# Optimization experiments

Measured on AMD Instinct MI355X. Metric: run time of the kernel, lower is better.

## Reference

```python
import jax, jax.numpy as jnp
import numpy as np

N_NODES = 50000


def _add_self_loops(edge_index, num_nodes):
    loop = jnp.arange(num_nodes, dtype=edge_index.dtype)
    row = jnp.concatenate([edge_index[0], loop])
    col = jnp.concatenate([edge_index[1], loop])
    return row, col


def _gcn_norm(row, col, num_nodes):
    # deg computed on target index with unit edge weights (PyG gcn_norm)
    deg = jax.ops.segment_sum(jnp.ones_like(col, dtype=jnp.float32), col,
                              num_segments=num_nodes)
    dis = jnp.where(deg > 0, jax.lax.rsqrt(jnp.maximum(deg, 1.0)), 0.0)
    return dis[row] * dis[col]  # [E]


def _gcn_conv(x, W, b, row, col, norm, num_nodes):
    h = x @ W                                  # dense transform first (PyG order)
    msg = h[row] * norm[:, None]               # gather + normalize
    out = jax.ops.segment_sum(msg, col, num_segments=num_nodes)  # scatter-add
    return out + b


def setup_inputs() -> dict:
    key = jax.random.key(0)
    ks = jax.random.split(key, 10)
    E = 800000
    x = jax.random.normal(ks[0], (N_NODES, 29), dtype=jnp.float32)
    edge_index = jax.random.randint(ks[1], (2, E), 0, N_NODES, dtype=jnp.int64)

    def glorot(k, fan_in, fan_out):
        s = jnp.sqrt(2.0 / (fan_in + fan_out)).astype(jnp.float32)
        return jax.random.normal(k, (fan_in, fan_out), dtype=jnp.float32) * s

    return {
        "x": x, "edge_index": edge_index,
        "W1": glorot(ks[2], 29, 96),  "b1": jnp.zeros((96,), jnp.float32),
        "W2": glorot(ks[3], 96, 128), "b2": jnp.zeros((128,), jnp.float32),
        "W3": glorot(ks[4], 128, 64), "b3": jnp.zeros((64,), jnp.float32),
        "W4": glorot(ks[5], 64, 32),  "b4": jnp.zeros((32,), jnp.float32),
    }


def reference(x, edge_index, W1, b1, W2, b2, W3, b3, W4, b4):
    row, col = _add_self_loops(edge_index, N_NODES)
    norm = _gcn_norm(row, col, N_NODES)  # same graph -> same norm for all layers
    h = _gcn_conv(x, W1, b1, row, col, norm, N_NODES)
    h = jax.nn.relu(h)
    # dropout(p=0.4) is identity in eval mode
    h = _gcn_conv(h, W2, b2, row, col, norm, N_NODES)
    h = _gcn_conv(h, W3, b3, row, col, norm, N_NODES)
    h = _gcn_conv(h, W4, b4, row, col, norm, N_NODES)
    return h
```

## Files before the change

### kernel.cpp

```cpp
#include <hip/hip_runtime.h>


constexpr int NN  = 50000;
constexpr int CAP = 64;
constexpr int AGB = (NN * 8 + 255) / 256;
constexpr int C1B = (NN + 255) / 256;
constexpr int PREPB = (NN * 32 + 64 + 255) / 256;
constexpr int W34XB = 17;
constexpr int W234XB = 13;
constexpr int PGB = 128;
constexpr int SLICE = (800000 + PGB - 1) / PGB;

typedef unsigned short u16;

__global__ void place_x_kernel(const int* __restrict__ row, const int* __restrict__ col,
                               int* __restrict__ cnt, u16* __restrict__ ell, int E) {
    const int g  = blockIdx.x & 7;
    const int bi = blockIdx.x >> 3;
    const int e0 = bi * SLICE;
    int e1 = e0 + SLICE; if (e1 > E) e1 = E;
    for (int e = e0 + threadIdx.x; e < e1; e += 256) {
        const int c = col[e];
        if ((unsigned)c >= (unsigned)NN || ((c >> 6) & 7) != g) continue;
        const int r = row[e];
        if ((unsigned)r >= (unsigned)NN) continue;
        const int pos = atomicAdd(&cnt[c], 1);
        if (pos < CAP) ell[c * CAP + pos] = (u16)r;
    }
}

__global__ void prep_all_kernel(const int* __restrict__ cnt, u16* __restrict__ ell,
                                const float* __restrict__ x, float* __restrict__ dis,
                                float* __restrict__ Ba, float* __restrict__ Bb,
                                float* __restrict__ c1d,
                                const float* __restrict__ W3, const float* __restrict__ W4,
                                const float* __restrict__ b3,
                                float* __restrict__ W34, float* __restrict__ v1) {
    if (blockIdx.x >= PREPB) {
        const int wid = (blockIdx.x - PREPB) * 256 + threadIdx.x;
        if (wid < 4096) {
            const int r = wid >> 5, j = wid & 31;
            float a = 0.f;
#pragma unroll 8
            for (int k = 0; k < 64; ++k) a = fmaf(W3[r * 64 + k], W4[k * 32 + j], a);
            W34[wid] = a;
        } else if (wid < 4128) {
            const int j = wid - 4096;
            float a = 0.f;
#pragma unroll 8
            for (int k = 0; k < 64; ++k) a = fmaf(b3[k], W4[k * 32 + j], a);
            v1[j] = a;
        }
        return;
    }
    const int idx = blockIdx.x * blockDim.x + threadIdx.x;
    if (idx < NN * 32) {
        const int n = idx >> 5, f = idx & 31;
        int m = cnt[n]; if (m > CAP) m = CAP;
        const float d = rsqrtf((float)m + 1.0f);
        Ba[idx] = (f < 29) ? x[n * 29 + f] * d : 0.f;
        if (f == 31) dis[n] = d;
        if (f == 30) {
            int mp = (m + 7) & ~7; if (mp > CAP) mp = CAP;
            for (int k = m; k < mp; ++k) ell[n * CAP + k] = (u16)NN;
        }
    } else {
        const int i = idx - NN * 32;
        if (i < 32) { Ba[NN * 32 + i] = 0.f; Bb[NN * 32 + i] = 0.f; }
        else if (i == 32) dis[NN] = 0.f;
        else if (i == 33) c1d[NN] = 0.f;
    }
}

template<int MODE>
__device__ __forceinline__ void agg32_body(const float* __restrict__ hs,
                                           const int* __restrict__ cnt,
                                           const u16* __restrict__ ell,
                                           const float* __restrict__ dis,
                                           const float* __restrict__ c1,
                                           const float* __restrict__ c2,
                                           const float* __restrict__ v1,
                                           const float* __restrict__ v2,
                                           const float* __restrict__ bv,
                                           float* __restrict__ out) {
    const int idx = blockIdx.x * blockDim.x + threadIdx.x;
    if (idx >= NN * 8) return;
    const int n = idx >> 3, c = idx & 7;
    const float4* hpc = (const float4*)hs + c;
    float4 acc = hpc[n * 8];
    int m = cnt[n]; if (m > CAP) m = CAP;
    const int m8 = (m + 7) >> 3;
    const int4* ip = (const int4*)(ell + (size_t)n * CAP);
    int t = 0;
    for (; t + 2 <= m8; t += 2) {
        const int4 sA = ip[t], sB = ip[t + 1];
        const unsigned ax = (unsigned)sA.x, ay = (unsigned)sA.y;
        const unsigned az = (unsigned)sA.z, aw = (unsigned)sA.w;
        const unsigned bx = (unsigned)sB.x, by = (unsigned)sB.y;
        const unsigned bz = (unsigned)sB.z, bw = (unsigned)sB.w;
        const float4 g0 = hpc[(ax & 0xFFFFu) * 8], g1 = hpc[(ax >> 16) * 8];
        const float4 g2 = hpc[(ay & 0xFFFFu) * 8], g3 = hpc[(ay >> 16) * 8];
        const float4 g4 = hpc[(az & 0xFFFFu) * 8], g5 = hpc[(az >> 16) * 8];
        const float4 g6 = hpc[(aw & 0xFFFFu) * 8], g7 = hpc[(aw >> 16) * 8];
        const float4 h0 = hpc[(bx & 0xFFFFu) * 8], h1 = hpc[(bx >> 16) * 8];
        const float4 h2 = hpc[(by & 0xFFFFu) * 8], h3 = hpc[(by >> 16) * 8];
        const float4 h4 = hpc[(bz & 0xFFFFu) * 8], h5 = hpc[(bz >> 16) * 8];
        const float4 h6 = hpc[(bw & 0xFFFFu) * 8], h7 = hpc[(bw >> 16) * 8];
        acc.x += (((g0.x + g1.x) + (g2.x + g3.x)) + ((g4.x + g5.x) + (g6.x + g7.x)))
               + (((h0.x + h1.x) + (h2.x + h3.x)) + ((h4.x + h5.x) + (h6.x + h7.x)));
        acc.y += (((g0.y + g1.y) + (g2.y + g3.y)) + ((g4.y + g5.y) + (g6.y + g7.y)))
               + (((h0.y + h1.y) + (h2.y + h3.y)) + ((h4.y + h5.y) + (h6.y + h7.y)));
        acc.z += (((g0.z + g1.z) + (g2.z + g3.z)) + ((g4.z + g5.z) + (g6.z + g7.z)))
               + (((h0.z + h1.z) + (h2.z + h3.z)) + ((h4.z + h5.z) + (h6.z + h7.z)));
        acc.w += (((g0.w + g1.w) + (g2.w + g3.w)) + ((g4.w + g5.w) + (g6.w + g7.w)))
               + (((h0.w + h1.w) + (h2.w + h3.w)) + ((h4.w + h5.w) + (h6.w + h7.w)));
    }
    if (t < m8) {
        const int4 s = ip[t];
        const unsigned ux = (unsigned)s.x, uy = (unsigned)s.y;
        const unsigned uz = (unsigned)s.z, uw = (unsigned)s.w;
        const float4 g0 = hpc[(ux & 0xFFFFu) * 8], g1 = hpc[(ux >> 16) * 8];
        const float4 g2 = hpc[(uy & 0xFFFFu) * 8], g3 = hpc[(uy >> 16) * 8];
        const float4 g4 = hpc[(uz & 0xFFFFu) * 8], g5 = hpc[(uz >> 16) * 8];
        const float4 g6 = hpc[(uw & 0xFFFFu) * 8], g7 = hpc[(uw >> 16) * 8];
        acc.x += ((g0.x + g1.x) + (g2.x + g3.x)) + ((g4.x + g5.x) + (g6.x + g7.x));
        acc.y += ((g0.y + g1.y) + (g2.y + g3.y)) + ((g4.y + g5.y) + (g6.y + g7.y));
        acc.z += ((g0.z + g1.z) + (g2.z + g3.z)) + ((g4.z + g5.z) + (g6.z + g7.z));
        acc.w += ((g0.w + g1.w) + (g2.w + g3.w)) + ((g4.w + g5.w) + (g6.w + g7.w));
    }
    const float d = dis[n];
    float4 r;
    if (MODE == 0) {
        r.x = acc.x * d; r.y = acc.y * d; r.z = acc.z * d; r.w = acc.w * d;
    } else if (MODE == 1) {
        const float d2 = d * d;
        r.x = acc.x * d2; r.y = acc.y * d2; r.z = acc.z * d2; r.w = acc.w * d2;
    } else {
        const float a1 = c1[n], a2 = c2[n];
        const float4 w1 = ((const float4*)v1)[c];
        const float4 w2 = ((const float4*)v2)[c];
        const float4 bb = ((const float4*)bv)[c];
        r.x = fmaf(acc.x, d, fmaf(a1, w1.x, fmaf(a2, w2.x, bb.x)));
        r.y = fmaf(acc.y, d, fmaf(a1, w1.y, fmaf(a2, w2.y, bb.y)));
        r.z = fmaf(acc.z, d, fmaf(a1, w1.z, fmaf(a2, w2.z, bb.z)));
        r.w = fmaf(acc.w, d, fmaf(a1, w1.w, fmaf(a2, w2.w, bb.w)));
    }
    ((float4*)out)[idx] = r;
}

__device__ __forceinline__ void agg1_body(const float* __restrict__ in,
                                          const int* __restrict__ cnt,
                                          const u16* __restrict__ ell,
                                          const float* __restrict__ dis,
                                          float* __restrict__ out,
                                          float* __restrict__ outd, int blk0) {
    const int n = (blockIdx.x - blk0) * 256 + threadIdx.x;
    if (n >= NN) return;
    float acc = in[n];
    int m = cnt[n]; if (m > CAP) m = CAP;
    const int m8 = (m + 7) >> 3;
    const int4* ip = (const int4*)(ell + (size_t)n * CAP);
    for (int t = 0; t < m8; ++t) {
        const int4 s = ip[t];
        const unsigned ux = (unsigned)s.x, uy = (unsigned)s.y;
        const unsigned uz = (unsigned)s.z, uw = (unsigned)s.w;
        acc += ((in[ux & 0xFFFFu] + in[ux >> 16]) + (in[uy & 0xFFFFu] + in[uy >> 16]))
             + ((in[uz & 0xFFFFu] + in[uz >> 16]) + (in[uw & 0xFFFFu] + in[uw >> 16]));
    }
    const float r = dis[n] * acc;
    out[n] = r;
    if (outd) outd[n] = r * dis[n];
}

__global__ void agg_pre_kernel(const float* __restrict__ Ba, const int* __restrict__ cnt,
                               const u16* __restrict__ ell, const float* __restrict__ dis,
                               float* __restrict__ Bb, float* __restrict__ c1,
                               float* __restrict__ c1d,
                               const float* __restrict__ W2, const float* __restrict__ b2,
                               const float* __restrict__ W34, float* __restrict__ W234,
                               float* __restrict__ v2) {
    if (blockIdx.x < AGB) {
        agg32_body<0>(Ba, cnt, ell, dis, nullptr, nullptr, nullptr, nullptr, nullptr, Bb);
    } else if (blockIdx.x < AGB + C1B) {
        agg1_body(dis, cnt, ell, dis, c1, c1d, AGB);
    } else {
        const int wid = (blockIdx.x - AGB - C1B) * 256 + threadIdx.x;
        if (wid < 3072) {
            const int r = wid >> 5, j = wid & 31;
            float a = 0.f;
#pragma unroll 8
            for (int k = 0; k < 128; ++k) a = fmaf(W2[r * 128 + k], W34[k * 32 + j], a);
            W234[wid] = a;
        } else if (wid < 3104) {
            const int j = wid - 3072;
            float a = 0.f;
#pragma unroll 8
            for (int k = 0; k < 128; ++k) a = fmaf(b2[k], W34[k * 32 + j], a);
            v2[j] = a;
        }
    }
}

__global__ void agg_hop1_kernel(const float* __restrict__ Ba, const int* __restrict__ cnt,
                                const u16* __restrict__ ell, const float* __restrict__ dis,
                                float* __restrict__ Bb, const float* __restrict__ c1d,
                                float* __restrict__ c2) {
    if (blockIdx.x < AGB)
        agg32_body<1>(Ba, cnt, ell, dis, nullptr, nullptr, nullptr, nullptr, nullptr, Bb);
    else
        agg1_body(c1d, cnt, ell, dis, c2, nullptr, AGB);
}

__global__ void agg_hop2_kernel(const float* __restrict__ Bb, const int* __restrict__ cnt,
                                const u16* __restrict__ ell, const float* __restrict__ dis,
                                float* __restrict__ Ba) {
    agg32_body<1>(Bb, cnt, ell, dis, nullptr, nullptr, nullptr, nullptr, nullptr, Ba);
}

__global__ void agg_hop3_kernel(const float* __restrict__ Ba, const int* __restrict__ cnt,
                                const u16* __restrict__ ell, const float* __restrict__ dis,
                                const float* __restrict__ c1, const float* __restrict__ c2,
                                const float* __restrict__ v1, const float* __restrict__ v2,
                                const float* __restrict__ bv, float* __restrict__ out) {
    agg32_body<2>(Ba, cnt, ell, dis, c1, c2, v1, v2, bv, out);
}

__global__ void __launch_bounds__(192, 2)
gemm_fused_kernel(const float* __restrict__ X, const float* __restrict__ W1,
                  const float* __restrict__ b1, const float* __restrict__ dis,
                  const float* __restrict__ W234, float* __restrict__ G) {
    constexpr int NPB = 16, RSX = 36, RSH = 104;
    __shared__ float xs[NPB * RSX];
    __shared__ float hsm[NPB * RSH];
    const int tid = threadIdx.x;
    const int n0  = blockIdx.x * NPB;

    const float4* Xv = (const float4*)(X + (size_t)n0 * 32);
    for (int i = tid; i < NPB * 8; i += 192) {
        const int nl = i >> 3, r = i & 7;
        float4 v = make_float4(0.f, 0.f, 0.f, 0.f);
        if (n0 + nl < NN) v = Xv[nl * 8 + r];
        *(float4*)(xs + nl * RSX + r * 4) = v;
    }
    __syncthreads();

    {
        const int cg = tid % 24, g = tid / 24;
        const float* x0 = xs + (2 * g) * RSX;
        const float* x1 = x0 + RSX;
        const float4* Wv = (const float4*)W1;
        float4 a0 = make_float4(0.f, 0.f, 0.f, 0.f);
        float4 a1 = make_float4(0.f, 0.f, 0.f, 0.f);
#pragma unroll
        for (int k = 0; k < 29; ++k) {
            const float4 w = Wv[k * 24 + cg];
            const float v0 = x0[k], v1 = x1[k];
            a0.x = fmaf(v0, w.x, a0.x); a0.y = fmaf(v0, w.y, a0.y);
            a0.z = fmaf(v0, w.z, a0.z); a0.w = fmaf(v0, w.w, a0.w);
            a1.x = fmaf(v1, w.x, a1.x); a1.y = fmaf(v1, w.y, a1.y);
            a1.z = fmaf(v1, w.z, a1.z); a1.w = fmaf(v1, w.w, a1.w);
        }
        const float4 bb = ((const float4*)b1)[cg];
#pragma unroll
        for (int h = 0; h < 2; ++h) {
            const int nl = 2 * g + h, node = n0 + nl;
            const float d = (node < NN) ? dis[node] : 0.f;
            const float4 a = h ? a1 : a0;
            float4 r;
            r.x = fmaxf(a.x + bb.x, 0.f) * d; r.y = fmaxf(a.y + bb.y, 0.f) * d;
            r.z = fmaxf(a.z + bb.z, 0.f) * d; r.w = fmaxf(a.w + bb.w, 0.f) * d;
            *(float4*)(hsm + nl * RSH + cg * 4) = r;
        }
    }
    __syncthreads();

    if (tid < 128) {
        const int nl = tid >> 3, cg = tid & 7;
        const float* hr = hsm + nl * RSH;
        const float4* Wv = (const float4*)W234;
        float4 a = make_float4(0.f, 0.f, 0.f, 0.f);
#pragma unroll 8
        for (int k = 0; k < 96; ++k) {
            const float4 w = Wv[k * 8 + cg];
            const float v = hr[k];
            a.x = fmaf(v, w.x, a.x); a.y = fmaf(v, w.y, a.y);
            a.z = fmaf(v, w.z, a.z); a.w = fmaf(v, w.w, a.w);
        }
        const int node = n0 + nl;
        if (node < NN) ((float4*)(G + (size_t)node * 32))[cg] = a;
    }
}

extern "C" void kernel_launch(void* const* d_in, const int* in_sizes, int n_in,
                              void* d_out, int out_size, void* d_ws, size_t ws_size,
                              hipStream_t stream) {
    const float* x  = (const float*)d_in[0];
    const int*   ei = (const int*)d_in[1];
    const float* W1 = (const float*)d_in[2]; const float* b1 = (const float*)d_in[3];
    const float* W2 = (const float*)d_in[4]; const float* b2 = (const float*)d_in[5];
    const float* W3 = (const float*)d_in[6]; const float* b3 = (const float*)d_in[7];
    const float* W4 = (const float*)d_in[8]; const float* b4p = (const float*)d_in[9];
    float* outp = (float*)d_out;

    const int E = in_sizes[1] / 2;
    const int* row = ei;
    const int* col = ei + E;

    int*   cnt  = (int*)d_ws;
    float* dis  = (float*)(cnt + 50048);
    u16*   ell  = (u16*)(dis + 50056);
    float* c1   = (float*)((int*)ell + 1600000);
    float* c1d  = c1 + 50056;
    float* c2   = c1d + 50056;
    float* W34  = c2 + 50056;
    float* W234 = W34 + 4096;
    float* v1   = W234 + 3072;
    float* v2   = v1 + 32;
    float* Ba   = v2 + 32;
    float* Bb   = Ba + 1600064;

    hipMemsetAsync(cnt, 0, 50048 * sizeof(int), stream);
    place_x_kernel<<<8 * PGB, 256, 0, stream>>>(row, col, cnt, ell, E);
    prep_all_kernel<<<PREPB + W34XB, 256, 0, stream>>>(cnt, ell, x, dis, Ba, Bb, c1d,
                                                       W3, W4, b3, W34, v1);
    agg_pre_kernel<<<AGB + C1B + W234XB, 256, 0, stream>>>(Ba, cnt, ell, dis, Bb, c1, c1d,
                                                           W2, b2, W34, W234, v2);
    gemm_fused_kernel<<<(NN + 15) / 16, 192, 0, stream>>>(Bb, W1, b1, dis, W234, Ba);
    agg_hop1_kernel<<<AGB + C1B, 256, 0, stream>>>(Ba, cnt, ell, dis, Bb, c1d, c2);
    agg_hop2_kernel<<<AGB, 256, 0, stream>>>(Bb, cnt, ell, dis, Ba);
    agg_hop3_kernel<<<AGB, 256, 0, stream>>>(Ba, cnt, ell, dis, c1, c2, v1, v2, b4p, outp);
}
```

Before: 221.9 us.

## Fuse first aggregation into GEMM kernel and shift weight precompute earlier

Moves the first 32-wide aggregation of x into the GEMM kernel, so each block gathers neighbour rows straight into shared memory. This removes one kernel launch and the round trip of the aggregated intermediate through global memory. The W3·W4 product moves into the placement kernel and W2·W34 into the prep kernel, so the pipeline keeps its dependency order with one fewer stage. In exchange, the GEMM kernel now carries the irregular gather latency, and only 128 of its 192 threads do the gather.

```diff
diff --git a/kernel.cpp b/kernel.cpp
--- a/kernel.cpp
+++ b/kernel.cpp
@@ -4,7 +4,9 @@
 constexpr int NN  = 50000;
 constexpr int CAP = 64;
 constexpr int AGB = (NN * 8 + 255) / 256;
+constexpr int AGGB = (NN + 15) / 16;
 constexpr int C1B = (NN + 255) / 256;
+constexpr int C1BF = (NN + 191) / 192;
 constexpr int PREPB = (NN * 32 + 64 + 255) / 256;
 constexpr int W34XB = 17;
 constexpr int W234XB = 13;
@@ -14,7 +16,27 @@
 typedef unsigned short u16;
 
 __global__ void place_x_kernel(const int* __restrict__ row, const int* __restrict__ col,
-                               int* __restrict__ cnt, u16* __restrict__ ell, int E) {
+                               int* __restrict__ cnt, u16* __restrict__ ell, int E,
+                               const float* __restrict__ W3, const float* __restrict__ W4,
+                               const float* __restrict__ b3,
+                               float* __restrict__ W34, float* __restrict__ v1) {
+    if (blockIdx.x >= 8 * PGB) {
+        const int wid = (blockIdx.x - 8 * PGB) * 256 + threadIdx.x;
+        if (wid < 4096) {
+            const int r = wid >> 5, j = wid & 31;
+            float a = 0.f;
+#pragma unroll 8
+            for (int k = 0; k < 64; ++k) a = fmaf(W3[r * 64 + k], W4[k * 32 + j], a);
+            W34[wid] = a;
+        } else if (wid < 4128) {
+            const int j = wid - 4096;
+            float a = 0.f;
+#pragma unroll 8
+            for (int k = 0; k < 64; ++k) a = fmaf(b3[k], W4[k * 32 + j], a);
+            v1[j] = a;
+        }
+        return;
+    }
     const int g  = blockIdx.x & 7;
     const int bi = blockIdx.x >> 3;
     const int e0 = bi * SLICE;
@@ -33,23 +55,23 @@
                                 const float* __restrict__ x, float* __restrict__ dis,
                                 float* __restrict__ Ba, float* __restrict__ Bb,
                                 float* __restrict__ c1d,
-                                const float* __restrict__ W3, const float* __restrict__ W4,
-                                const float* __restrict__ b3,
-                                float* __restrict__ W34, float* __restrict__ v1) {
+                                const float* __restrict__ W2, const float* __restrict__ b2,
+                                const float* __restrict__ W34,
+                                float* __restrict__ W234, float* __restrict__ v2) {
     if (blockIdx.x >= PREPB) {
         const int wid = (blockIdx.x - PREPB) * 256 + threadIdx.x;
-        if (wid < 4096) {
+        if (wid < 3072) {
             const int r = wid >> 5, j = wid & 31;
             float a = 0.f;
 #pragma unroll 8
-            for (int k = 0; k < 64; ++k) a = fmaf(W3[r * 64 + k], W4[k * 32 + j], a);
-            W34[wid] = a;
-        } else if (wid < 4128) {
-            const int j = wid - 4096;
+            for (int k = 0; k < 128; ++k) a = fmaf(W2[r * 128 + k], W34[k * 32 + j], a);
+            W234[wid] = a;
+        } else if (wid < 3104) {
+            const int j = wid - 3072;
             float a = 0.f;
 #pragma unroll 8
-            for (int k = 0; k < 64; ++k) a = fmaf(b3[k], W4[k * 32 + j], a);
-            v1[j] = a;
+            for (int k = 0; k < 128; ++k) a = fmaf(b2[k], W34[k * 32 + j], a);
+            v2[j] = a;
         }
         return;
     }
@@ -130,9 +152,7 @@
     }
     const float d = dis[n];
     float4 r;
-    if (MODE == 0) {
-        r.x = acc.x * d; r.y = acc.y * d; r.z = acc.z * d; r.w = acc.w * d;
-    } else if (MODE == 1) {
+    if (MODE == 1) {
         const float d2 = d * d;
         r.x = acc.x * d2; r.y = acc.y * d2; r.z = acc.z * d2; r.w = acc.w * d2;
     } else {
@@ -153,8 +173,9 @@
                                           const u16* __restrict__ ell,
                                           const float* __restrict__ dis,
                                           float* __restrict__ out,
-                                          float* __restrict__ outd, int blk0) {
-    const int n = (blockIdx.x - blk0) * 256 + threadIdx.x;
+                                          float* __restrict__ outd,
+                                          int blk0, int bsz) {
+    const int n = (blockIdx.x - blk0) * bsz + threadIdx.x;
     if (n >= NN) return;
     float acc = in[n];
     int m = cnt[n]; if (m > CAP) m = CAP;
@@ -172,75 +193,49 @@
     if (outd) outd[n] = r * dis[n];
 }
 
-__global__ void agg_pre_kernel(const float* __restrict__ Ba, const int* __restrict__ cnt,
-                               const u16* __restrict__ ell, const float* __restrict__ dis,
-                               float* __restrict__ Bb, float* __restrict__ c1,
-                               float* __restrict__ c1d,
-                               const float* __restrict__ W2, const float* __restrict__ b2,
-                               const float* __restrict__ W34, float* __restrict__ W234,
-                               float* __restrict__ v2) {
-    if (blockIdx.x < AGB) {
-        agg32_body<0>(Ba, cnt, ell, dis, nullptr, nullptr, nullptr, nullptr, nullptr, Bb);
-    } else if (blockIdx.x < AGB + C1B) {
-        agg1_body(dis, cnt, ell, dis, c1, c1d, AGB);
-    } else {
-        const int wid = (blockIdx.x - AGB - C1B) * 256 + threadIdx.x;
-        if (wid < 3072) {
-            const int r = wid >> 5, j = wid & 31;
-            float a = 0.f;
-#pragma unroll 8
-            for (int k = 0; k < 128; ++k) a = fmaf(W2[r * 128 + k], W34[k * 32 + j], a);
-            W234[wid] = a;
-        } else if (wid < 3104) {
-            const int j = wid - 3072;
-            float a = 0.f;
-#pragma unroll 8
-            for (int k = 0; k < 128; ++k) a = fmaf(b2[k], W34[k * 32 + j], a);
-            v2[j] = a;
-        }
-    }
-}
-
-__global__ void agg_hop1_kernel(const float* __restrict__ Ba, const int* __restrict__ cnt,
-                                const u16* __restrict__ ell, const float* __restrict__ dis,
-                                float* __restrict__ Bb, const float* __restrict__ c1d,
-                                float* __restrict__ c2) {
-    if (blockIdx.x < AGB)
-        agg32_body<1>(Ba, cnt, ell, dis, nullptr, nullptr, nullptr, nullptr, nullptr, Bb);
-    else
-        agg1_body(c1d, cnt, ell, dis, c2, nullptr, AGB);
-}
-
-__global__ void agg_hop2_kernel(const float* __restrict__ Bb, const int* __restrict__ cnt,
-                                const u16* __restrict__ ell, const float* __restrict__ dis,
-                                float* __restrict__ Ba) {
-    agg32_body<1>(Bb, cnt, ell, dis, nullptr, nullptr, nullptr, nullptr, nullptr, Ba);
-}
-
-__global__ void agg_hop3_kernel(const float* __restrict__ Ba, const int* __restrict__ cnt,
-                                const u16* __restrict__ ell, const float* __restrict__ dis,
-                                const float* __restrict__ c1, const float* __restrict__ c2,
-                                const float* __restrict__ v1, const float* __restrict__ v2,
-                                const float* __restrict__ bv, float* __restrict__ out) {
-    agg32_body<2>(Ba, cnt, ell, dis, c1, c2, v1, v2, bv, out);
-}
-
 __global__ void __launch_bounds__(192, 2)
-gemm_fused_kernel(const float* __restrict__ X, const float* __restrict__ W1,
-                  const float* __restrict__ b1, const float* __restrict__ dis,
-                  const float* __restrict__ W234, float* __restrict__ G) {
+agg_gemm_kernel(const float* __restrict__ Ba, const int* __restrict__ cnt,
+                const u16* __restrict__ ell, const float* __restrict__ dis,
+                const float* __restrict__ W1, const float* __restrict__ b1,
+                const float* __restrict__ W234, float* __restrict__ G,
+                float* __restrict__ c1, float* __restrict__ c1d) {
+    if (blockIdx.x >= AGGB) {
+        agg1_body(dis, cnt, ell, dis, c1, c1d, AGGB, 192);
+        return;
+    }
     constexpr int NPB = 16, RSX = 36, RSH = 104;
     __shared__ float xs[NPB * RSX];
     __shared__ float hsm[NPB * RSH];
     const int tid = threadIdx.x;
     const int n0  = blockIdx.x * NPB;
 
-    const float4* Xv = (const float4*)(X + (size_t)n0 * 32);
-    for (int i = tid; i < NPB * 8; i += 192) {
-        const int nl = i >> 3, r = i & 7;
-        float4 v = make_float4(0.f, 0.f, 0.f, 0.f);
-        if (n0 + nl < NN) v = Xv[nl * 8 + r];
-        *(float4*)(xs + nl * RSX + r * 4) = v;
+    if (tid < 128) {
+        const int nl = tid >> 3, c = tid & 7;
+        const int n = n0 + nl;
+        float4 r = make_float4(0.f, 0.f, 0.f, 0.f);
+        if (n < NN) {
+            const float4* hpc = (const float4*)Ba + c;
+            float4 acc = hpc[n * 8];
+            int m = cnt[n]; if (m > CAP) m = CAP;
+            const int m8 = (m + 7) >> 3;
+            const int4* ip = (const int4*)(ell + (size_t)n * CAP);
+            for (int t = 0; t < m8; ++t) {
+                const int4 s = ip[t];
+                const unsigned ux = (unsigned)s.x, uy = (unsigned)s.y;
+                const unsigned uz = (unsigned)s.z, uw = (unsigned)s.w;
+                const float4 g0 = hpc[(ux & 0xFFFFu) * 8], g1 = hpc[(ux >> 16) * 8];
+                const float4 g2 = hpc[(uy & 0xFFFFu) * 8], g3 = hpc[(uy >> 16) * 8];
+                const float4 g4 = hpc[(uz & 0xFFFFu) * 8], g5 = hpc[(uz >> 16) * 8];
+                const float4 g6 = hpc[(uw & 0xFFFFu) * 8], g7 = hpc[(uw >> 16) * 8];
+                acc.x += ((g0.x + g1.x) + (g2.x + g3.x)) + ((g4.x + g5.x) + (g6.x + g7.x));
+                acc.y += ((g0.y + g1.y) + (g2.y + g3.y)) + ((g4.y + g5.y) + (g6.y + g7.y));
+                acc.z += ((g0.z + g1.z) + (g2.z + g3.z)) + ((g4.z + g5.z) + (g6.z + g7.z));
+                acc.w += ((g0.w + g1.w) + (g2.w + g3.w)) + ((g4.w + g5.w) + (g6.w + g7.w));
+            }
+            const float d = dis[n];
+            r.x = acc.x * d; r.y = acc.y * d; r.z = acc.z * d; r.w = acc.w * d;
+        }
+        *(float4*)(xs + nl * RSX + c * 4) = r;
     }
     __syncthreads();
 
@@ -291,6 +286,30 @@
     }
 }
 
+__global__ void agg_hop1_kernel(const float* __restrict__ Bb, const int* __restrict__ cnt,
+                                const u16* __restrict__ ell, const float* __restrict__ dis,
+                                float* __restrict__ Ba, const float* __restrict__ c1d,
+                                float* __restrict__ c2) {
+    if (blockIdx.x < AGB)
+        agg32_body<1>(Bb, cnt, ell, dis, nullptr, nullptr, nullptr, nullptr, nullptr, Ba);
+    else
+        agg1_body(c1d, cnt, ell, dis, c2, nullptr, AGB, 256);
+}
+
+__global__ void agg_hop2_kernel(const float* __restrict__ Ba, const int* __restrict__ cnt,
+                                const u16* __restrict__ ell, const float* __restrict__ dis,
+                                float* __restrict__ Bb) {
+    agg32_body<1>(Ba, cnt, ell, dis, nullptr, nullptr, nullptr, nullptr, nullptr, Bb);
+}
+
+__global__ void agg_hop3_kernel(const float* __restrict__ Bb, const int* __restrict__ cnt,
+                                const u16* __restrict__ ell, const float* __restrict__ dis,
+                                const float* __restrict__ c1, const float* __restrict__ c2,
+                                const float* __restrict__ v1, const float* __restrict__ v2,
+                                const float* __restrict__ bv, float* __restrict__ out) {
+    agg32_body<2>(Bb, cnt, ell, dis, c1, c2, v1, v2, bv, out);
+}
+
 extern "C" void kernel_launch(void* const* d_in, const int* in_sizes, int n_in,
                               void* d_out, int out_size, void* d_ws, size_t ws_size,
                               hipStream_t stream) {
@@ -320,13 +339,13 @@
     float* Bb   = Ba + 1600064;
 
     hipMemsetAsync(cnt, 0, 50048 * sizeof(int), stream);
-    place_x_kernel<<<8 * PGB, 256, 0, stream>>>(row, col, cnt, ell, E);
-    prep_all_kernel<<<PREPB + W34XB, 256, 0, stream>>>(cnt, ell, x, dis, Ba, Bb, c1d,
-                                                       W3, W4, b3, W34, v1);
-    agg_pre_kernel<<<AGB + C1B + W234XB, 256, 0, stream>>>(Ba, cnt, ell, dis, Bb, c1, c1d,
-                                                           W2, b2, W34, W234, v2);
-    gemm_fused_kernel<<<(NN + 15) / 16, 192, 0, stream>>>(Bb, W1, b1, dis, W234, Ba);
-    agg_hop1_kernel<<<AGB + C1B, 256, 0, stream>>>(Ba, cnt, ell, dis, Bb, c1d, c2);
-    agg_hop2_kernel<<<AGB, 256, 0, stream>>>(Bb, cnt, ell, dis, Ba);
-    agg_hop3_kernel<<<AGB, 256, 0, stream>>>(Ba, cnt, ell, dis, c1, c2, v1, v2, b4p, outp);
-}
+    place_x_kernel<<<8 * PGB + W34XB, 256, 0, stream>>>(row, col, cnt, ell, E,
+                                                        W3, W4, b3, W34, v1);
+    prep_all_kernel<<<PREPB + W234XB, 256, 0, stream>>>(cnt, ell, x, dis, Ba, Bb, c1d,
+                                                        W2, b2, W34, W234, v2);
+    agg_gemm_kernel<<<AGGB + C1BF, 192, 0, stream>>>(Ba, cnt, ell, dis,
+                                                     W1, b1, W234, Bb, c1, c1d);
+    agg_hop1_kernel<<<AGB + C1B, 256, 0, stream>>>(Bb, cnt, ell, dis, Ba, c1d, c2);
+    agg_hop2_kernel<<<AGB, 256, 0, stream>>>(Ba, cnt, ell, dis, Bb);
+    agg_hop3_kernel<<<AGB, 256, 0, stream>>>(Bb, cnt, ell, dis, c1, c2, v1, v2, b4p, outp);
+}
```

New measurement: 222.4 us. Within noise of the previous version (+0.3%).
